# Optimization experiments

Hardware: AMD Instinct MI355X
Metric: run time of the kernel (lower is better)

## Reference

```python
import jax, jax.numpy as jnp
from jax import lax
import numpy as np

B, IN, OUT = 32768, 512, 512


def _bit_length(a):
    # a: nonnegative int32. Smear high bit down, then popcount == bit length.
    y = a
    y = y | (y >> 1)
    y = y | (y >> 2)
    y = y | (y >> 4)
    y = y | (y >> 8)
    y = y | (y >> 16)
    return lax.population_count(y)


def trunc_top_bits(v, k=4):
    # compress_top4(|a|,|b|,4): keep top-k significant bits of each magnitude.
    a = jnp.abs(v)
    shift = jnp.maximum(_bit_length(a) - k, 0)
    t = (a >> shift) << shift
    return t * jnp.sign(v)


def setup_inputs() -> dict:
    key = jax.random.key(0)
    k1, k2, k3 = jax.random.split(key, 3)
    bound = 1.0 / np.sqrt(IN)  # matches kaiming_uniform(a=sqrt(5)) + bias bound
    x = jax.random.normal(k1, (B, IN), dtype=jnp.float32)
    weight = jax.random.uniform(k2, (OUT, IN), dtype=jnp.float32, minval=-bound, maxval=bound)
    bias = jax.random.uniform(k3, (OUT,), dtype=jnp.float32, minval=-bound, maxval=bound)
    return {"x": x, "weight": weight, "bias": bias, "weight_sf": 8, "act_sf": 6}


def reference(x, weight, bias, weight_sf, act_sf):
    # Fixed-point quantization: input / 2^{-sf} then trunc-toward-zero int cast
    xi = (x * (2.0 ** act_sf)).astype(jnp.int32)       # [B, IN]
    wi = (weight * (2.0 ** weight_sf)).astype(jnp.int32)  # [OUT, IN]
    # sign/abs decomposition + top-4-bit truncated multiply-accumulate:
    # sum_y compress_top4(|xi|,|wi|) * sign(xi)*sign(wi) == dot of signed truncs
    tx = trunc_top_bits(xi).astype(jnp.float32)
    tw = trunc_top_bits(wi).astype(jnp.float32)
    acc = jnp.einsum("bi,oi->bo", tx, tw)             # [B, OUT], exact in fp32
    scale = (2.0 ** (-act_sf)) * (2.0 ** (-weight_sf))
    return acc * scale + bias[None, :]
```

## Files before the change

### kernel.cpp

```cpp
#include <hip/hip_runtime.h>
#include <hip/hip_bf16.h>
#include <stdint.h>

#define B_DIM 32768
#define IN_DIM 512
#define OUT_DIM 512

typedef __bf16 bf16;
typedef bf16 bf16x8 __attribute__((ext_vector_type(8)));
typedef float f32x4 __attribute__((ext_vector_type(4)));

__device__ __forceinline__ float quant_trunc(float v, float scale) {
    int xi = (int)(v * scale);
    int a  = xi < 0 ? -xi : xi;
    int bl = a ? (32 - __builtin_clz((unsigned)a)) : 0;
    int sh = bl > 4 ? bl - 4 : 0;
    int t  = (a >> sh) << sh;
    return (float)(xi < 0 ? -t : t);
}

__global__ void quant_kernel(const float* __restrict__ in, bf16* __restrict__ out,
                             int n4, const int* __restrict__ sf) {
    int i = blockIdx.x * blockDim.x + threadIdx.x;
    if (i >= n4) return;
    float scale = (float)(1 << *sf);
    float4 v = ((const float4*)in)[i];
    union { bf16 h[4]; uint2 u; } cv;
    cv.h[0] = (bf16)quant_trunc(v.x, scale);
    cv.h[1] = (bf16)quant_trunc(v.y, scale);
    cv.h[2] = (bf16)quant_trunc(v.z, scale);
    cv.h[3] = (bf16)quant_trunc(v.w, scale);
    ((uint2*)out)[i] = cv.u;
}

__global__ __launch_bounds__(256)
void gemm_bt(const bf16* __restrict__ A, const bf16* __restrict__ W,
             const float* __restrict__ bias, float* __restrict__ C,
             const int* __restrict__ wsf, const int* __restrict__ asf) {
    __shared__ bf16 As[128 * 64];
    __shared__ bf16 Bs[128 * 64];

    const int t    = threadIdx.x;
    const int w    = t >> 6;
    const int lane = t & 63;
    const int bm   = blockIdx.x >> 2;
    const int bn   = blockIdx.x & 3;
    const int row0 = bm * 128;
    const int col0 = bn * 128;
    const int wm   = (w & 1) * 64;
    const int wn   = (w >> 1) * 64;

    const int ldr = t >> 3;
    const int ldc = (t & 7) * 8;

    const bf16* Abase = A + (size_t)row0 * IN_DIM;
    const bf16* Wbase = W + (size_t)col0 * IN_DIM;

    f32x4 acc[4][4];
    for (int mt = 0; mt < 4; ++mt)
        for (int nt = 0; nt < 4; ++nt)
            acc[mt][nt] = 0.0f;

    for (int k0 = 0; k0 < IN_DIM; k0 += 64) {
        #pragma unroll
        for (int i = 0; i < 4; ++i) {
            const bf16* ga = Abase + (size_t)(i * 32 + ldr) * IN_DIM + k0 + ldc;
            bf16*       la = As + i * 2048 + w * 512;
            __builtin_amdgcn_global_load_lds((const __attribute__((address_space(1))) void*)ga,
                                             (__attribute__((address_space(3))) void*)la, 16, 0, 0);
            const bf16* gb = Wbase + (size_t)(i * 32 + ldr) * IN_DIM + k0 + ldc;
            bf16*       lb = Bs + i * 2048 + w * 512;
            __builtin_amdgcn_global_load_lds((const __attribute__((address_space(1))) void*)gb,
                                             (__attribute__((address_space(3))) void*)lb, 16, 0, 0);
        }
        __syncthreads();

        #pragma unroll
        for (int ks = 0; ks < 2; ++ks) {
            const int kcol = ks * 32 + (lane >> 4) * 8;
            const int arow = wm + (lane & 15);
            const int brow = wn + (lane & 15);
            bf16x8 af[4], bf[4];
            #pragma unroll
            for (int mt = 0; mt < 4; ++mt)
                af[mt] = *(const bf16x8*)(As + (arow + mt * 16) * 64 + kcol);
            #pragma unroll
            for (int nt = 0; nt < 4; ++nt)
                bf[nt] = *(const bf16x8*)(Bs + (brow + nt * 16) * 64 + kcol);
            #pragma unroll
            for (int mt = 0; mt < 4; ++mt)
                #pragma unroll
                for (int nt = 0; nt < 4; ++nt)
                    acc[mt][nt] = __builtin_amdgcn_mfma_f32_16x16x32_bf16(af[mt], bf[nt], acc[mt][nt], 0, 0, 0);
        }
        __syncthreads();
    }

    const float oscale = ldexpf(1.0f, -(*wsf + *asf));
    const int cl = lane & 15;
    const int rg = (lane >> 4) * 4;
    #pragma unroll
    for (int nt = 0; nt < 4; ++nt) {
        const int col = col0 + wn + nt * 16 + cl;
        const float bv = bias[col];
        #pragma unroll
        for (int mt = 0; mt < 4; ++mt) {
            f32x4 a = acc[mt][nt];
            #pragma unroll
            for (int r = 0; r < 4; ++r) {
                const int row = row0 + wm + mt * 16 + rg + r;
                C[(size_t)row * OUT_DIM + col] = a[r] * oscale + bv;
            }
        }
    }
}

extern "C" void kernel_launch(void* const* d_in, const int* in_sizes, int n_in,
                              void* d_out, int out_size, void* d_ws, size_t ws_size,
                              hipStream_t stream) {
    const float* x    = (const float*)d_in[0];
    const float* wgt  = (const float*)d_in[1];
    const float* bias = (const float*)d_in[2];
    const int*   wsf  = (const int*)d_in[3];
    const int*   asf  = (const int*)d_in[4];

    bf16* tx = (bf16*)d_ws;
    bf16* tw = (bf16*)((char*)d_ws + (size_t)B_DIM * IN_DIM * sizeof(bf16));

    const int nx4 = B_DIM * IN_DIM / 4;
    const int nw4 = OUT_DIM * IN_DIM / 4;
    quant_kernel<<<(nx4 + 255) / 256, 256, 0, stream>>>(x, tx, nx4, asf);
    quant_kernel<<<(nw4 + 255) / 256, 256, 0, stream>>>(wgt, tw, nw4, wsf);

    const int grid = (B_DIM / 128) * (OUT_DIM / 128);
    gemm_bt<<<grid, 256, 0, stream>>>(tx, tw, bias, (float*)d_out, wsf, asf);
}
```

Measured before the change: 151.6 us.

## Fuse activation quantization into GEMM A-tile load and remap blocks per XCD

Removes the separate activation quantization pass: the GEMM now reads fp32 activations directly, quantizes them in registers, and stores bf16 into shared memory. This drops the extra write and read of a 32 MB bf16 intermediate. The top-4-bit truncation becomes a bit mask on the float representation. Block indices are remapped so each XCD handles a contiguous row range that shares the same X rows, and launch bounds request 4 blocks per CU. The tradeoff is that A loads become synchronous register loads instead of direct-to-LDS loads, so the GEMM reads twice as many bytes per A tile and adds ALU work in its load phase.

```diff
diff --git a/kernel.cpp b/kernel.cpp
--- a/kernel.cpp
+++ b/kernel.cpp
@@ -10,13 +10,10 @@
 typedef bf16 bf16x8 __attribute__((ext_vector_type(8)));
 typedef float f32x4 __attribute__((ext_vector_type(4)));
 
-__device__ __forceinline__ float quant_trunc(float v, float scale) {
-    int xi = (int)(v * scale);
-    int a  = xi < 0 ? -xi : xi;
-    int bl = a ? (32 - __builtin_clz((unsigned)a)) : 0;
-    int sh = bl > 4 ? bl - 4 : 0;
-    int t  = (a >> sh) << sh;
-    return (float)(xi < 0 ? -t : t);
+__device__ __forceinline__ uint32_t quant2(float a, float b, float scale) {
+    uint32_t ua = __float_as_uint(truncf(a * scale)) & 0xFFF00000u;
+    uint32_t ub = __float_as_uint(truncf(b * scale)) & 0xFFF00000u;
+    return (ua >> 16) | (ub & 0xFFFF0000u);
 }
 
 __global__ void quant_kernel(const float* __restrict__ in, bf16* __restrict__ out,
@@ -25,26 +22,28 @@
     if (i >= n4) return;
     float scale = (float)(1 << *sf);
     float4 v = ((const float4*)in)[i];
-    union { bf16 h[4]; uint2 u; } cv;
-    cv.h[0] = (bf16)quant_trunc(v.x, scale);
-    cv.h[1] = (bf16)quant_trunc(v.y, scale);
-    cv.h[2] = (bf16)quant_trunc(v.z, scale);
-    cv.h[3] = (bf16)quant_trunc(v.w, scale);
-    ((uint2*)out)[i] = cv.u;
+    uint2 p;
+    p.x = quant2(v.x, v.y, scale);
+    p.y = quant2(v.z, v.w, scale);
+    ((uint2*)out)[i] = p;
 }
 
-__global__ __launch_bounds__(256)
-void gemm_bt(const bf16* __restrict__ A, const bf16* __restrict__ W,
-             const float* __restrict__ bias, float* __restrict__ C,
-             const int* __restrict__ wsf, const int* __restrict__ asf) {
+__global__ __launch_bounds__(256, 4)
+void gemm_fused(const float* __restrict__ X, const bf16* __restrict__ QW,
+                const float* __restrict__ bias, float* __restrict__ C,
+                const int* __restrict__ wsf, const int* __restrict__ asf) {
     __shared__ bf16 As[128 * 64];
     __shared__ bf16 Bs[128 * 64];
 
     const int t    = threadIdx.x;
     const int w    = t >> 6;
     const int lane = t & 63;
-    const int bm   = blockIdx.x >> 2;
-    const int bn   = blockIdx.x & 3;
+
+    const int b    = blockIdx.x;
+    const int xcd  = b & 7;
+    const int slot = b >> 3;
+    const int bm   = xcd * 32 + (slot >> 2);
+    const int bn   = slot & 3;
     const int row0 = bm * 128;
     const int col0 = bn * 128;
     const int wm   = (w & 1) * 64;
@@ -53,8 +52,10 @@
     const int ldr = t >> 3;
     const int ldc = (t & 7) * 8;
 
-    const bf16* Abase = A + (size_t)row0 * IN_DIM;
-    const bf16* Wbase = W + (size_t)col0 * IN_DIM;
+    const float* Xbase = X  + (size_t)row0 * IN_DIM;
+    const bf16*  Wbase = QW + (size_t)col0 * IN_DIM;
+
+    const float ascale = (float)(1 << *asf);
 
     f32x4 acc[4][4];
     for (int mt = 0; mt < 4; ++mt)
@@ -64,14 +65,22 @@
     for (int k0 = 0; k0 < IN_DIM; k0 += 64) {
         #pragma unroll
         for (int i = 0; i < 4; ++i) {
-            const bf16* ga = Abase + (size_t)(i * 32 + ldr) * IN_DIM + k0 + ldc;
-            bf16*       la = As + i * 2048 + w * 512;
-            __builtin_amdgcn_global_load_lds((const __attribute__((address_space(1))) void*)ga,
-                                             (__attribute__((address_space(3))) void*)la, 16, 0, 0);
             const bf16* gb = Wbase + (size_t)(i * 32 + ldr) * IN_DIM + k0 + ldc;
             bf16*       lb = Bs + i * 2048 + w * 512;
             __builtin_amdgcn_global_load_lds((const __attribute__((address_space(1))) void*)gb,
                                              (__attribute__((address_space(3))) void*)lb, 16, 0, 0);
+        }
+        #pragma unroll
+        for (int i = 0; i < 4; ++i) {
+            const float* g = Xbase + (size_t)(i * 32 + ldr) * IN_DIM + k0 + ldc;
+            float4 v0 = ((const float4*)g)[0];
+            float4 v1 = ((const float4*)g)[1];
+            uint4 p;
+            p.x = quant2(v0.x, v0.y, ascale);
+            p.y = quant2(v0.z, v0.w, ascale);
+            p.z = quant2(v1.x, v1.y, ascale);
+            p.w = quant2(v1.z, v1.w, ascale);
+            *(uint4*)(As + (i * 32 + ldr) * 64 + ldc) = p;
         }
         __syncthreads();
 
@@ -124,14 +133,11 @@
     const int*   wsf  = (const int*)d_in[3];
     const int*   asf  = (const int*)d_in[4];
 
-    bf16* tx = (bf16*)d_ws;
-    bf16* tw = (bf16*)((char*)d_ws + (size_t)B_DIM * IN_DIM * sizeof(bf16));
+    bf16* tw = (bf16*)d_ws;
 
-    const int nx4 = B_DIM * IN_DIM / 4;
     const int nw4 = OUT_DIM * IN_DIM / 4;
-    quant_kernel<<<(nx4 + 255) / 256, 256, 0, stream>>>(x, tx, nx4, asf);
     quant_kernel<<<(nw4 + 255) / 256, 256, 0, stream>>>(wgt, tw, nw4, wsf);
 
     const int grid = (B_DIM / 128) * (OUT_DIM / 128);
-    gemm_bt<<<grid, 256, 0, stream>>>(tx, tw, bias, (float*)d_out, wsf, asf);
+    gemm_fused<<<grid, 256, 0, stream>>>(x, tw, bias, (float*)d_out, wsf, asf);
 }
```

Measured after the change: 157.7 us. 4.0% more time.
